# Kernel optimization log

Hardware: AMD Instinct MI355X
Metric: run time of the kernel (lower is better)

The kernel has to match this reference:

```python
import jax, jax.numpy as jnp
import numpy as np

MEM_DIM = 256
NUM_CHILDREN = 16
BATCH = 16384


def setup_inputs() -> dict:
    key = jax.random.key(0)
    k1, k2, k3, k4, k5, k6 = jax.random.split(key, 6)
    D = MEM_DIM
    s = 1.0 / np.sqrt(D)
    return {
        "children_memory": jax.random.normal(k1, (NUM_CHILDREN, BATCH, D), jnp.float32),
        "children_hidden": jax.random.normal(k2, (NUM_CHILDREN, BATCH, D), jnp.float32),
        "Wf": jax.random.normal(k3, (D, D), jnp.float32) * s,
        "bf": jax.random.normal(k4, (D,), jnp.float32) * s,
        "Wiou": jax.random.normal(k5, (3 * D, D), jnp.float32) * s,
        "biou": jax.random.normal(k6, (3 * D,), jnp.float32) * s,
    }


def reference(children_memory, children_hidden, Wf, bf, Wiou, biou):
    D = Wf.shape[0]
    # sum of children hidden states over the child axis -> [B, D]
    hidden_sum = jnp.sum(children_hidden, axis=0)
    # per-child forget gates: [C, B, D]
    forget_gates = jax.nn.sigmoid(jnp.einsum("cbd,ed->cbe", children_hidden, Wf) + bf)
    # i/o/u gates from summed hidden: [B, 3D]
    iou = jnp.einsum("bd,ed->be", hidden_sum, Wiou) + biou
    input_gate = jax.nn.sigmoid(iou[:, :D])
    output_gate = jax.nn.sigmoid(iou[:, D:2 * D])
    memory_gate = jnp.tanh(iou[:, 2 * D:])
    node_memory = input_gate * memory_gate + jnp.sum(forget_gates * children_memory, axis=0)
    node_hidden = output_gate * jnp.tanh(node_memory)
    return node_memory, node_hidden
```

## Files before the change

kernel.cpp:

```cpp
#include <hip/hip_runtime.h>
#include <hip/hip_bf16.h>

#define CC 16
#define BB 16384
#define DD 256
#define BT 16
#define NT 512
#define SLAB ((size_t)BB * DD)

typedef float f32x4 __attribute__((ext_vector_type(4)));
typedef short bf16x8 __attribute__((ext_vector_type(8)));
typedef short bf16x4 __attribute__((ext_vector_type(4)));

static __device__ __forceinline__ short bfc(float f) {
    return (short)__builtin_bit_cast(unsigned short, __float2bfloat16(f));
}
static __device__ __forceinline__ bf16x8 pack8(f32x4 a, f32x4 b) {
    bf16x8 v;
    v[0] = bfc(a[0]); v[1] = bfc(a[1]); v[2] = bfc(a[2]); v[3] = bfc(a[3]);
    v[4] = bfc(b[0]); v[5] = bfc(b[1]); v[6] = bfc(b[2]); v[7] = bfc(b[3]);
    return v;
}
static __device__ __forceinline__ float sigm(float x) {
    return __builtin_amdgcn_rcpf(1.0f + __expf(-x));
}
static __device__ __forceinline__ float tanh_(float x) {
    return 2.0f * __builtin_amdgcn_rcpf(1.0f + __expf(-2.0f * x)) - 1.0f;
}

__global__ void prep(const float* __restrict__ Wf, const float* __restrict__ Wiou,
                     short* __restrict__ ws) {
    const int row = blockIdx.x;
    const int t   = threadIdx.x;
    const float* src = (row < 256) ? (Wf + (size_t)row * DD)
                                   : (Wiou + (size_t)(row - 256) * DD);
    f32x4 v = *(const f32x4*)(src + t * 4);
    bf16x4 o; o[0] = bfc(v[0]); o[1] = bfc(v[1]); o[2] = bfc(v[2]); o[3] = bfc(v[3]);
    *(bf16x4*)(ws + (size_t)row * DD + t * 4) = o;
}

__global__ __launch_bounds__(NT, 2) void treelstm(
    const float* __restrict__ cmem,
    const float* __restrict__ chid,
    const short* __restrict__ wpk,
    const float* __restrict__ bfv,
    const float* __restrict__ biou,
    float* __restrict__ out)
{
    __shared__ __align__(64) unsigned char hb[2][2][BT * DD * 2];

    const int tid  = threadIdx.x;
    const int lane = tid & 63;
    const int wid  = tid >> 6;
    const int l15  = lane & 15;
    const int l4   = lane >> 4;
    const int b0   = blockIdx.x * BT;
    const int wc0  = wid * 32;
    const int swr  = l15 << 4;

    const int srow   = tid >> 5;
    const int schunk = tid & 31;
    const float* hg  = chid + (size_t)(b0 + srow) * DD + schunk * 8;
    const int wb     = srow * 512 + (((schunk ^ srow) & 31) << 4);

    f32x4 hA0 = *(const f32x4*)(hg);
    f32x4 hA1 = *(const f32x4*)(hg + 4);
    f32x4 hA2 = *(const f32x4*)(hg + SLAB);
    f32x4 hA3 = *(const f32x4*)(hg + SLAB + 4);

    bf16x8 wfr[2][8];
    float bfr[2];
#pragma unroll
    for (int n = 0; n < 2; ++n) {
        const short* wr = wpk + (size_t)(wc0 + n * 16 + l15) * DD + l4 * 8;
#pragma unroll
        for (int k = 0; k < 8; ++k) wfr[n][k] = *(const bf16x8*)(wr + k * 32);
        bfr[n] = bfv[wc0 + n * 16 + l15];
    }

    const float* cmp = cmem + (size_t)(b0 + l4 * 4) * DD + wc0 + l15;
    float cmE[8], cmO[8];
#pragma unroll
    for (int n = 0; n < 2; ++n)
#pragma unroll
        for (int j = 0; j < 4; ++j) cmE[n * 4 + j] = cmp[j * DD + n * 16];

    float hs[8], nmv[8];
#pragma unroll
    for (int i = 0; i < 8; ++i) { hs[i] = 0.f; nmv[i] = 0.f; }

#pragma unroll
    for (int i = 0; i < 4; ++i) {
        hs[i] += hA0[i] + hA2[i];
        hs[4 + i] += hA1[i] + hA3[i];
    }
    *(bf16x8*)(&hb[0][0][0] + wb) = pack8(hA0, hA1);
    *(bf16x8*)(&hb[0][1][0] + wb) = pack8(hA2, hA3);
    asm volatile("s_waitcnt lgkmcnt(0)" ::: "memory");
    __builtin_amdgcn_s_barrier();
    __builtin_amdgcn_sched_barrier(0);

    const float* hgn = hg + 2 * SLAB;
    const float* cmn = cmp + SLAB;

#pragma unroll 1
    for (int P = 0; P < 8; ++P) {
        if (P < 7) {
            hA0 = *(const f32x4*)(hgn);
            hA1 = *(const f32x4*)(hgn + 4);
            hA2 = *(const f32x4*)(hgn + SLAB);
            hA3 = *(const f32x4*)(hgn + SLAB + 4);
            hgn += 2 * SLAB;
        }
#pragma unroll
        for (int n = 0; n < 2; ++n)
#pragma unroll
            for (int j = 0; j < 4; ++j) cmO[n * 4 + j] = cmn[j * DD + n * 16];
        cmn += SLAB;

        f32x4 e0 = {bfr[0], bfr[0], bfr[0], bfr[0]};
        f32x4 e1 = {bfr[1], bfr[1], bfr[1], bfr[1]};
        f32x4 e2 = {0.f, 0.f, 0.f, 0.f}, e3 = {0.f, 0.f, 0.f, 0.f};
        const unsigned char* bcE = &hb[P & 1][0][0] + l15 * 512;
#pragma unroll
        for (int kk = 0; kk < 4; ++kk) {
            bf16x8 a = *(const bf16x8*)(bcE + ((((kk) << 6) + (l4 << 4)) ^ swr));
            e0 = __builtin_amdgcn_mfma_f32_16x16x32_bf16(a, wfr[0][kk], e0, 0, 0, 0);
            e1 = __builtin_amdgcn_mfma_f32_16x16x32_bf16(a, wfr[1][kk], e1, 0, 0, 0);
        }
#pragma unroll
        for (int kk = 4; kk < 8; ++kk) {
            bf16x8 a = *(const bf16x8*)(bcE + ((((kk) << 6) + (l4 << 4)) ^ swr));
            e2 = __builtin_amdgcn_mfma_f32_16x16x32_bf16(a, wfr[0][kk], e2, 0, 0, 0);
            e3 = __builtin_amdgcn_mfma_f32_16x16x32_bf16(a, wfr[1][kk], e3, 0, 0, 0);
        }
#pragma unroll
        for (int j = 0; j < 4; ++j) {
            nmv[j]     += sigm(e0[j] + e2[j]) * cmE[j];
            nmv[4 + j] += sigm(e1[j] + e3[j]) * cmE[4 + j];
        }
        if (P < 7) {
#pragma unroll
            for (int n = 0; n < 2; ++n)
#pragma unroll
                for (int j = 0; j < 4; ++j) cmE[n * 4 + j] = cmn[j * DD + n * 16];
        }
        cmn += SLAB;

        f32x4 o0 = {bfr[0], bfr[0], bfr[0], bfr[0]};
        f32x4 o1 = {bfr[1], bfr[1], bfr[1], bfr[1]};
        f32x4 o2 = {0.f, 0.f, 0.f, 0.f}, o3 = {0.f, 0.f, 0.f, 0.f};
        const unsigned char* bcO = &hb[P & 1][1][0] + l15 * 512;
#pragma unroll
        for (int kk = 0; kk < 4; ++kk) {
            bf16x8 a = *(const bf16x8*)(bcO + ((((kk) << 6) + (l4 << 4)) ^ swr));
            o0 = __builtin_amdgcn_mfma_f32_16x16x32_bf16(a, wfr[0][kk], o0, 0, 0, 0);
            o1 = __builtin_amdgcn_mfma_f32_16x16x32_bf16(a, wfr[1][kk], o1, 0, 0, 0);
        }
#pragma unroll
        for (int kk = 4; kk < 8; ++kk) {
            bf16x8 a = *(const bf16x8*)(bcO + ((((kk) << 6) + (l4 << 4)) ^ swr));
            o2 = __builtin_amdgcn_mfma_f32_16x16x32_bf16(a, wfr[0][kk], o2, 0, 0, 0);
            o3 = __builtin_amdgcn_mfma_f32_16x16x32_bf16(a, wfr[1][kk], o3, 0, 0, 0);
        }

        if (P < 7) {
#pragma unroll
            for (int i = 0; i < 4; ++i) {
                hs[i] += hA0[i] + hA2[i];
                hs[4 + i] += hA1[i] + hA3[i];
            }
            *(bf16x8*)(&hb[(P & 1) ^ 1][0][0] + wb) = pack8(hA0, hA1);
            *(bf16x8*)(&hb[(P & 1) ^ 1][1][0] + wb) = pack8(hA2, hA3);
            asm volatile("s_waitcnt lgkmcnt(0)" ::: "memory");
            __builtin_amdgcn_s_barrier();
            __builtin_amdgcn_sched_barrier(0);
        }

#pragma unroll
        for (int j = 0; j < 4; ++j) {
            nmv[j]     += sigm(o0[j] + o2[j]) * cmO[j];
            nmv[4 + j] += sigm(o1[j] + o3[j]) * cmO[4 + j];
        }
    }

    {
        f32x4 s0 = {hs[0], hs[1], hs[2], hs[3]};
        f32x4 s1 = {hs[4], hs[5], hs[6], hs[7]};
        *(bf16x8*)(&hb[0][0][0] + wb) = pack8(s0, s1);
    }
    asm volatile("s_waitcnt lgkmcnt(0)" ::: "memory");
    __builtin_amdgcn_s_barrier();
    __builtin_amdgcn_sched_barrier(0);

    bf16x8 afr[8];
    {
        const unsigned char* bc = &hb[0][0][0] + l15 * 512;
#pragma unroll
        for (int kk = 0; kk < 8; ++kk)
            afr[kk] = *(const bf16x8*)(bc + (((kk << 6) + (l4 << 4)) ^ swr));
    }

    float gq[3][8];
#pragma unroll
    for (int q = 0; q < 3; ++q) {
#pragma unroll
        for (int n = 0; n < 2; ++n) {
            const short* wr = wpk + (size_t)(256 + q * 256 + wc0 + n * 16 + l15) * DD + l4 * 8;
            f32x4 acc = {0.f, 0.f, 0.f, 0.f};
#pragma unroll
            for (int kk = 0; kk < 8; ++kk)
                acc = __builtin_amdgcn_mfma_f32_16x16x32_bf16(afr[kk], *(const bf16x8*)(wr + kk * 32), acc, 0, 0, 0);
            float bq = biou[q * 256 + wc0 + n * 16 + l15];
#pragma unroll
            for (int j = 0; j < 4; ++j) gq[q][n * 4 + j] = acc[j] + bq;
        }
    }

    float* o0p = out + (size_t)(b0 + l4 * 4) * DD + wc0 + l15;
    float* o1p = o0p + SLAB;
#pragma unroll
    for (int n = 0; n < 2; ++n)
#pragma unroll
        for (int j = 0; j < 4; ++j) {
            float ig = sigm(gq[0][n * 4 + j]);
            float og = sigm(gq[1][n * 4 + j]);
            float ug = tanh_(gq[2][n * 4 + j]);
            float mm = nmv[n * 4 + j] + ig * ug;
            float hh = og * tanh_(mm);
            o0p[j * DD + n * 16] = mm;
            o1p[j * DD + n * 16] = hh;
        }
}

extern "C" void kernel_launch(void* const* d_in, const int* in_sizes, int n_in,
                              void* d_out, int out_size, void* d_ws, size_t ws_size,
                              hipStream_t stream) {
    const float* cmem = (const float*)d_in[0];
    const float* chid = (const float*)d_in[1];
    const float* Wf   = (const float*)d_in[2];
    const float* bf   = (const float*)d_in[3];
    const float* Wiou = (const float*)d_in[4];
    const float* biou = (const float*)d_in[5];
    float* out = (float*)d_out;
    short* wpk = (short*)d_ws;

    prep<<<1024, 64, 0, stream>>>(Wf, Wiou, wpk);
    treelstm<<<BB / BT, NT, 0, stream>>>(cmem, chid, wpk, bf, biou, out);
}
```

Measured before the change: 165.1 us.

## Split output columns across two blocks per batch tile with 256 threads

Each batch tile of 16 rows is now processed by two blocks, each covering 128 of the 256 output columns with 4 waves instead of 8. Each block still stages the full hidden rows into shared memory, so children_hidden reads are duplicated across the pair. The odd-child hidden load is deferred to mid-iteration to reduce live registers. The aim is more blocks and occupancy flexibility, at the cost of doubled hidden-state traffic unless L2 absorbs it.

```diff
diff --git a/kernel.cpp b/kernel.cpp
--- a/kernel.cpp
+++ b/kernel.cpp
@@ -5,7 +5,7 @@
 #define BB 16384
 #define DD 256
 #define BT 16
-#define NT 512
+#define NT 256
 #define SLAB ((size_t)BB * DD)
 
 typedef float f32x4 __attribute__((ext_vector_type(4)));
@@ -54,83 +54,97 @@
     const int wid  = tid >> 6;
     const int l15  = lane & 15;
     const int l4   = lane >> 4;
-    const int b0   = blockIdx.x * BT;
-    const int wc0  = wid * 32;
-    const int swr  = l15 << 4;
-
-    const int srow   = tid >> 5;
-    const int schunk = tid & 31;
-    const float* hg  = chid + (size_t)(b0 + srow) * DD + schunk * 8;
-    const int wb     = srow * 512 + (((schunk ^ srow) & 31) << 4);
-
-    f32x4 hA0 = *(const f32x4*)(hg);
-    f32x4 hA1 = *(const f32x4*)(hg + 4);
-    f32x4 hA2 = *(const f32x4*)(hg + SLAB);
-    f32x4 hA3 = *(const f32x4*)(hg + SLAB + 4);
+    const int bx   = blockIdx.x;
+    const int b0   = (bx >> 1) * BT;
+    const int cbase = (bx & 1) * 128 + wid * 32;
+
+    const int srow = tid >> 4;
+    const int sfc  = (tid & 15) * 16;
+    const float* hg = chid + (size_t)(b0 + srow) * DD + sfc;
+    const int c0w = (tid & 15) * 2;
+    const int wb0 = srow * 512 + ((((c0w)     ^ srow) & 31) << 4);
+    const int wb1 = srow * 512 + ((((c0w + 1) ^ srow) & 31) << 4);
+
+    f32x4 hN0 = *(const f32x4*)(hg);
+    f32x4 hN1 = *(const f32x4*)(hg + 4);
+    f32x4 hN2 = *(const f32x4*)(hg + 8);
+    f32x4 hN3 = *(const f32x4*)(hg + 12);
+    f32x4 hO0 = *(const f32x4*)(hg + SLAB);
+    f32x4 hO1 = *(const f32x4*)(hg + SLAB + 4);
+    f32x4 hO2 = *(const f32x4*)(hg + SLAB + 8);
+    f32x4 hO3 = *(const f32x4*)(hg + SLAB + 12);
 
     bf16x8 wfr[2][8];
     float bfr[2];
 #pragma unroll
     for (int n = 0; n < 2; ++n) {
-        const short* wr = wpk + (size_t)(wc0 + n * 16 + l15) * DD + l4 * 8;
+        const short* wr = wpk + (size_t)(cbase + n * 16 + l15) * DD + l4 * 8;
 #pragma unroll
         for (int k = 0; k < 8; ++k) wfr[n][k] = *(const bf16x8*)(wr + k * 32);
-        bfr[n] = bfv[wc0 + n * 16 + l15];
-    }
-
-    const float* cmp = cmem + (size_t)(b0 + l4 * 4) * DD + wc0 + l15;
+        bfr[n] = bfv[cbase + n * 16 + l15];
+    }
+
+    const float* cmp = cmem + (size_t)(b0 + l4 * 4) * DD + cbase + l15;
     float cmE[8], cmO[8];
 #pragma unroll
     for (int n = 0; n < 2; ++n)
 #pragma unroll
         for (int j = 0; j < 4; ++j) cmE[n * 4 + j] = cmp[j * DD + n * 16];
 
-    float hs[8], nmv[8];
-#pragma unroll
-    for (int i = 0; i < 8; ++i) { hs[i] = 0.f; nmv[i] = 0.f; }
+    float hs[16], nmv[8];
+#pragma unroll
+    for (int i = 0; i < 16; ++i) hs[i] = 0.f;
+#pragma unroll
+    for (int i = 0; i < 8; ++i) nmv[i] = 0.f;
 
 #pragma unroll
     for (int i = 0; i < 4; ++i) {
-        hs[i] += hA0[i] + hA2[i];
-        hs[4 + i] += hA1[i] + hA3[i];
-    }
-    *(bf16x8*)(&hb[0][0][0] + wb) = pack8(hA0, hA1);
-    *(bf16x8*)(&hb[0][1][0] + wb) = pack8(hA2, hA3);
+        hs[i]      += hN0[i] + hO0[i];
+        hs[4 + i]  += hN1[i] + hO1[i];
+        hs[8 + i]  += hN2[i] + hO2[i];
+        hs[12 + i] += hN3[i] + hO3[i];
+    }
+    *(bf16x8*)(&hb[0][0][0] + wb0) = pack8(hN0, hN1);
+    *(bf16x8*)(&hb[0][0][0] + wb1) = pack8(hN2, hN3);
+    *(bf16x8*)(&hb[0][1][0] + wb0) = pack8(hO0, hO1);
+    *(bf16x8*)(&hb[0][1][0] + wb1) = pack8(hO2, hO3);
     asm volatile("s_waitcnt lgkmcnt(0)" ::: "memory");
     __builtin_amdgcn_s_barrier();
     __builtin_amdgcn_sched_barrier(0);
 
-    const float* hgn = hg + 2 * SLAB;
-    const float* cmn = cmp + SLAB;
+    const int swr = l15 << 4;
 
 #pragma unroll 1
     for (int P = 0; P < 8; ++P) {
+        const int par = P & 1;
         if (P < 7) {
-            hA0 = *(const f32x4*)(hgn);
-            hA1 = *(const f32x4*)(hgn + 4);
-            hA2 = *(const f32x4*)(hgn + SLAB);
-            hA3 = *(const f32x4*)(hgn + SLAB + 4);
-            hgn += 2 * SLAB;
-        }
-#pragma unroll
-        for (int n = 0; n < 2; ++n)
-#pragma unroll
-            for (int j = 0; j < 4; ++j) cmO[n * 4 + j] = cmn[j * DD + n * 16];
-        cmn += SLAB;
+            const float* hn = hg + (size_t)(2 * P + 2) * SLAB;
+            hN0 = *(const f32x4*)(hn);
+            hN1 = *(const f32x4*)(hn + 4);
+            hN2 = *(const f32x4*)(hn + 8);
+            hN3 = *(const f32x4*)(hn + 12);
+        }
+        {
+            const float* cn = cmp + (size_t)(2 * P + 1) * SLAB;
+#pragma unroll
+            for (int n = 0; n < 2; ++n)
+#pragma unroll
+                for (int j = 0; j < 4; ++j) cmO[n * 4 + j] = cn[j * DD + n * 16];
+        }
 
         f32x4 e0 = {bfr[0], bfr[0], bfr[0], bfr[0]};
         f32x4 e1 = {bfr[1], bfr[1], bfr[1], bfr[1]};
         f32x4 e2 = {0.f, 0.f, 0.f, 0.f}, e3 = {0.f, 0.f, 0.f, 0.f};
-        const unsigned char* bcE = &hb[P & 1][0][0] + l15 * 512;
+        const unsigned char* bcE = &hb[par][0][0] + l15 * 512;
 #pragma unroll
         for (int kk = 0; kk < 4; ++kk) {
-            bf16x8 a = *(const bf16x8*)(bcE + ((((kk) << 6) + (l4 << 4)) ^ swr));
+            bf16x8 a = *(const bf16x8*)(bcE + (((kk << 6) + (l4 << 4)) ^ swr));
             e0 = __builtin_amdgcn_mfma_f32_16x16x32_bf16(a, wfr[0][kk], e0, 0, 0, 0);
             e1 = __builtin_amdgcn_mfma_f32_16x16x32_bf16(a, wfr[1][kk], e1, 0, 0, 0);
         }
 #pragma unroll
         for (int kk = 4; kk < 8; ++kk) {
-            bf16x8 a = *(const bf16x8*)(bcE + ((((kk) << 6) + (l4 << 4)) ^ swr));
+            bf16x8 a = *(const bf16x8*)(bcE + (((kk << 6) + (l4 << 4)) ^ swr));
             e2 = __builtin_amdgcn_mfma_f32_16x16x32_bf16(a, wfr[0][kk], e2, 0, 0, 0);
             e3 = __builtin_amdgcn_mfma_f32_16x16x32_bf16(a, wfr[1][kk], e3, 0, 0, 0);
         }
@@ -139,27 +153,40 @@
             nmv[j]     += sigm(e0[j] + e2[j]) * cmE[j];
             nmv[4 + j] += sigm(e1[j] + e3[j]) * cmE[4 + j];
         }
+
         if (P < 7) {
 #pragma unroll
+            for (int i = 0; i < 4; ++i) {
+                hs[i] += hN0[i]; hs[4 + i] += hN1[i];
+                hs[8 + i] += hN2[i]; hs[12 + i] += hN3[i];
+            }
+            *(bf16x8*)(&hb[par ^ 1][0][0] + wb0) = pack8(hN0, hN1);
+            *(bf16x8*)(&hb[par ^ 1][0][0] + wb1) = pack8(hN2, hN3);
+            const float* ho = hg + (size_t)(2 * P + 3) * SLAB;
+            hO0 = *(const f32x4*)(ho);
+            hO1 = *(const f32x4*)(ho + 4);
+            hO2 = *(const f32x4*)(ho + 8);
+            hO3 = *(const f32x4*)(ho + 12);
+            const float* cn = cmp + (size_t)(2 * P + 2) * SLAB;
+#pragma unroll
             for (int n = 0; n < 2; ++n)
 #pragma unroll
-                for (int j = 0; j < 4; ++j) cmE[n * 4 + j] = cmn[j * DD + n * 16];
-        }
-        cmn += SLAB;
+                for (int j = 0; j < 4; ++j) cmE[n * 4 + j] = cn[j * DD + n * 16];
+        }
 
         f32x4 o0 = {bfr[0], bfr[0], bfr[0], bfr[0]};
         f32x4 o1 = {bfr[1], bfr[1], bfr[1], bfr[1]};
         f32x4 o2 = {0.f, 0.f, 0.f, 0.f}, o3 = {0.f, 0.f, 0.f, 0.f};
-        const unsigned char* bcO = &hb[P & 1][1][0] + l15 * 512;
+        const unsigned char* bcO = &hb[par][1][0] + l15 * 512;
 #pragma unroll
         for (int kk = 0; kk < 4; ++kk) {
-            bf16x8 a = *(const bf16x8*)(bcO + ((((kk) << 6) + (l4 << 4)) ^ swr));
+            bf16x8 a = *(const bf16x8*)(bcO + (((kk << 6) + (l4 << 4)) ^ swr));
             o0 = __builtin_amdgcn_mfma_f32_16x16x32_bf16(a, wfr[0][kk], o0, 0, 0, 0);
             o1 = __builtin_amdgcn_mfma_f32_16x16x32_bf16(a, wfr[1][kk], o1, 0, 0, 0);
         }
 #pragma unroll
         for (int kk = 4; kk < 8; ++kk) {
-            bf16x8 a = *(const bf16x8*)(bcO + ((((kk) << 6) + (l4 << 4)) ^ swr));
+            bf16x8 a = *(const bf16x8*)(bcO + (((kk << 6) + (l4 << 4)) ^ swr));
             o2 = __builtin_amdgcn_mfma_f32_16x16x32_bf16(a, wfr[0][kk], o2, 0, 0, 0);
             o3 = __builtin_amdgcn_mfma_f32_16x16x32_bf16(a, wfr[1][kk], o3, 0, 0, 0);
         }
@@ -167,11 +194,11 @@
         if (P < 7) {
 #pragma unroll
             for (int i = 0; i < 4; ++i) {
-                hs[i] += hA0[i] + hA2[i];
-                hs[4 + i] += hA1[i] + hA3[i];
+                hs[i] += hO0[i]; hs[4 + i] += hO1[i];
+                hs[8 + i] += hO2[i]; hs[12 + i] += hO3[i];
             }
-            *(bf16x8*)(&hb[(P & 1) ^ 1][0][0] + wb) = pack8(hA0, hA1);
-            *(bf16x8*)(&hb[(P & 1) ^ 1][1][0] + wb) = pack8(hA2, hA3);
+            *(bf16x8*)(&hb[par ^ 1][1][0] + wb0) = pack8(hO0, hO1);
+            *(bf16x8*)(&hb[par ^ 1][1][0] + wb1) = pack8(hO2, hO3);
             asm volatile("s_waitcnt lgkmcnt(0)" ::: "memory");
             __builtin_amdgcn_s_barrier();
             __builtin_amdgcn_sched_barrier(0);
@@ -187,7 +214,10 @@
     {
         f32x4 s0 = {hs[0], hs[1], hs[2], hs[3]};
         f32x4 s1 = {hs[4], hs[5], hs[6], hs[7]};
-        *(bf16x8*)(&hb[0][0][0] + wb) = pack8(s0, s1);
+        f32x4 s2 = {hs[8], hs[9], hs[10], hs[11]};
+        f32x4 s3 = {hs[12], hs[13], hs[14], hs[15]};
+        *(bf16x8*)(&hb[0][0][0] + wb0) = pack8(s0, s1);
+        *(bf16x8*)(&hb[0][0][0] + wb1) = pack8(s2, s3);
     }
     asm volatile("s_waitcnt lgkmcnt(0)" ::: "memory");
     __builtin_amdgcn_s_barrier();
@@ -206,18 +236,18 @@
     for (int q = 0; q < 3; ++q) {
 #pragma unroll
         for (int n = 0; n < 2; ++n) {
-            const short* wr = wpk + (size_t)(256 + q * 256 + wc0 + n * 16 + l15) * DD + l4 * 8;
+            const short* wr = wpk + (size_t)(256 + q * 256 + cbase + n * 16 + l15) * DD + l4 * 8;
             f32x4 acc = {0.f, 0.f, 0.f, 0.f};
 #pragma unroll
             for (int kk = 0; kk < 8; ++kk)
                 acc = __builtin_amdgcn_mfma_f32_16x16x32_bf16(afr[kk], *(const bf16x8*)(wr + kk * 32), acc, 0, 0, 0);
-            float bq = biou[q * 256 + wc0 + n * 16 + l15];
+            float bq = biou[q * 256 + cbase + n * 16 + l15];
 #pragma unroll
             for (int j = 0; j < 4; ++j) gq[q][n * 4 + j] = acc[j] + bq;
         }
     }
 
-    float* o0p = out + (size_t)(b0 + l4 * 4) * DD + wc0 + l15;
+    float* o0p = out + (size_t)(b0 + l4 * 4) * DD + cbase + l15;
     float* o1p = o0p + SLAB;
 #pragma unroll
     for (int n = 0; n < 2; ++n)
@@ -246,5 +276,5 @@
     short* wpk = (short*)d_ws;
 
     prep<<<1024, 64, 0, stream>>>(Wf, Wiou, wpk);
-    treelstm<<<BB / BT, NT, 0, stream>>>(cmem, chid, wpk, bf, biou, out);
-}
+    treelstm<<<(BB / BT) * 2, NT, 0, stream>>>(cmem, chid, wpk, bf, biou, out);
+}
```

Measured after the change: 169.0 us. +2.4%, slower.

## Load hidden A-fragments directly into registers and split columns across two blocks

Applied to the files above, without the earlier changes.

Replaces the LDS-staged, barrier-synchronised double buffer for child hidden states with direct per-wave global loads. Each wave now packs the full 16x256 bf16 A operand in registers and processes one child per iteration without any block barriers. The grid doubles, with each 256-thread block covering half the output columns. The price is that every wave, and both column-half blocks, re-read the same hidden tile, which relies on L1/L2 to absorb the redundant traffic. Register pressure also rises from holding 64 floats of prefetched hidden data.

```diff
diff --git a/kernel.cpp b/kernel.cpp
--- a/kernel.cpp
+++ b/kernel.cpp
@@ -4,8 +4,7 @@
 #define CC 16
 #define BB 16384
 #define DD 256
-#define BT 16
-#define NT 512
+#define NT 256
 #define SLAB ((size_t)BB * DD)
 
 typedef float f32x4 __attribute__((ext_vector_type(4)));
@@ -47,158 +46,121 @@
     const float* __restrict__ biou,
     float* __restrict__ out)
 {
-    __shared__ __align__(64) unsigned char hb[2][2][BT * DD * 2];
+    __shared__ float hsbuf[16][264];
 
     const int tid  = threadIdx.x;
     const int lane = tid & 63;
     const int wid  = tid >> 6;
     const int l15  = lane & 15;
     const int l4   = lane >> 4;
-    const int b0   = blockIdx.x * BT;
-    const int wc0  = wid * 32;
-    const int swr  = l15 << 4;
-
-    const int srow   = tid >> 5;
-    const int schunk = tid & 31;
-    const float* hg  = chid + (size_t)(b0 + srow) * DD + schunk * 8;
-    const int wb     = srow * 512 + (((schunk ^ srow) & 31) << 4);
-
-    f32x4 hA0 = *(const f32x4*)(hg);
-    f32x4 hA1 = *(const f32x4*)(hg + 4);
-    f32x4 hA2 = *(const f32x4*)(hg + SLAB);
-    f32x4 hA3 = *(const f32x4*)(hg + SLAB + 4);
+    const int bx   = blockIdx.x;
+    const int b0   = (bx >> 1) * 16;
+    const int cbase = (bx & 1) * 128 + wid * 32;
+
+    const float* hA = chid + (size_t)(b0 + l15) * DD + l4 * 8;
+
+    f32x4 hv[16];
+#pragma unroll
+    for (int kk = 0; kk < 8; ++kk) {
+        hv[2 * kk]     = *(const f32x4*)(hA + kk * 32);
+        hv[2 * kk + 1] = *(const f32x4*)(hA + kk * 32 + 4);
+    }
 
     bf16x8 wfr[2][8];
     float bfr[2];
 #pragma unroll
     for (int n = 0; n < 2; ++n) {
-        const short* wr = wpk + (size_t)(wc0 + n * 16 + l15) * DD + l4 * 8;
+        const short* wr = wpk + (size_t)(cbase + n * 16 + l15) * DD + l4 * 8;
 #pragma unroll
         for (int k = 0; k < 8; ++k) wfr[n][k] = *(const bf16x8*)(wr + k * 32);
-        bfr[n] = bfv[wc0 + n * 16 + l15];
-    }
-
-    const float* cmp = cmem + (size_t)(b0 + l4 * 4) * DD + wc0 + l15;
-    float cmE[8], cmO[8];
+        bfr[n] = bfv[cbase + n * 16 + l15];
+    }
+
+    const float* cmp = cmem + (size_t)(b0 + l4 * 4) * DD + cbase + l15;
+    float cmv[8];
 #pragma unroll
     for (int n = 0; n < 2; ++n)
 #pragma unroll
-        for (int j = 0; j < 4; ++j) cmE[n * 4 + j] = cmp[j * DD + n * 16];
-
-    float hs[8], nmv[8];
-#pragma unroll
-    for (int i = 0; i < 8; ++i) { hs[i] = 0.f; nmv[i] = 0.f; }
-
-#pragma unroll
-    for (int i = 0; i < 4; ++i) {
-        hs[i] += hA0[i] + hA2[i];
-        hs[4 + i] += hA1[i] + hA3[i];
-    }
-    *(bf16x8*)(&hb[0][0][0] + wb) = pack8(hA0, hA1);
-    *(bf16x8*)(&hb[0][1][0] + wb) = pack8(hA2, hA3);
-    asm volatile("s_waitcnt lgkmcnt(0)" ::: "memory");
-    __builtin_amdgcn_s_barrier();
-    __builtin_amdgcn_sched_barrier(0);
-
-    const float* hgn = hg + 2 * SLAB;
-    const float* cmn = cmp + SLAB;
+        for (int j = 0; j < 4; ++j) cmv[n * 4 + j] = cmp[j * DD + n * 16];
+
+    float hs[16], nmv[8];
+#pragma unroll
+    for (int i = 0; i < 16; ++i) hs[i] = 0.f;
+#pragma unroll
+    for (int i = 0; i < 8; ++i) nmv[i] = 0.f;
+
+    bf16x8 a[8];
 
 #pragma unroll 1
-    for (int P = 0; P < 8; ++P) {
-        if (P < 7) {
-            hA0 = *(const f32x4*)(hgn);
-            hA1 = *(const f32x4*)(hgn + 4);
-            hA2 = *(const f32x4*)(hgn + SLAB);
-            hA3 = *(const f32x4*)(hgn + SLAB + 4);
-            hgn += 2 * SLAB;
-        }
-#pragma unroll
-        for (int n = 0; n < 2; ++n)
-#pragma unroll
-            for (int j = 0; j < 4; ++j) cmO[n * 4 + j] = cmn[j * DD + n * 16];
-        cmn += SLAB;
-
-        f32x4 e0 = {bfr[0], bfr[0], bfr[0], bfr[0]};
-        f32x4 e1 = {bfr[1], bfr[1], bfr[1], bfr[1]};
-        f32x4 e2 = {0.f, 0.f, 0.f, 0.f}, e3 = {0.f, 0.f, 0.f, 0.f};
-        const unsigned char* bcE = &hb[P & 1][0][0] + l15 * 512;
-#pragma unroll
-        for (int kk = 0; kk < 4; ++kk) {
-            bf16x8 a = *(const bf16x8*)(bcE + ((((kk) << 6) + (l4 << 4)) ^ swr));
-            e0 = __builtin_amdgcn_mfma_f32_16x16x32_bf16(a, wfr[0][kk], e0, 0, 0, 0);
-            e1 = __builtin_amdgcn_mfma_f32_16x16x32_bf16(a, wfr[1][kk], e1, 0, 0, 0);
-        }
-#pragma unroll
-        for (int kk = 4; kk < 8; ++kk) {
-            bf16x8 a = *(const bf16x8*)(bcE + ((((kk) << 6) + (l4 << 4)) ^ swr));
-            e2 = __builtin_amdgcn_mfma_f32_16x16x32_bf16(a, wfr[0][kk], e2, 0, 0, 0);
-            e3 = __builtin_amdgcn_mfma_f32_16x16x32_bf16(a, wfr[1][kk], e3, 0, 0, 0);
-        }
+    for (int c = 0; c < CC; ++c) {
+#pragma unroll
+        for (int kk = 0; kk < 8; ++kk) {
+            if ((kk >> 1) == wid) {
+                const int half = (kk & 1) * 8;
+#pragma unroll
+                for (int i = 0; i < 4; ++i) {
+                    hs[half + i]     += hv[2 * kk][i];
+                    hs[half + 4 + i] += hv[2 * kk + 1][i];
+                }
+            }
+            a[kk] = pack8(hv[2 * kk], hv[2 * kk + 1]);
+        }
+
+        if (c + 1 < CC) {
+            const float* hn = hA + (size_t)(c + 1) * SLAB;
+#pragma unroll
+            for (int kk = 0; kk < 8; ++kk) {
+                hv[2 * kk]     = *(const f32x4*)(hn + kk * 32);
+                hv[2 * kk + 1] = *(const f32x4*)(hn + kk * 32 + 4);
+            }
+        }
+        float cmn[8];
+        if (c + 1 < CC) {
+            const float* cn = cmp + (size_t)(c + 1) * SLAB;
+#pragma unroll
+            for (int n = 0; n < 2; ++n)
+#pragma unroll
+                for (int j = 0; j < 4; ++j) cmn[n * 4 + j] = cn[j * DD + n * 16];
+        }
+
+        f32x4 acc0 = {bfr[0], bfr[0], bfr[0], bfr[0]};
+        f32x4 acc1 = {bfr[1], bfr[1], bfr[1], bfr[1]};
+#pragma unroll
+        for (int kk = 0; kk < 8; ++kk) {
+            acc0 = __builtin_amdgcn_mfma_f32_16x16x32_bf16(a[kk], wfr[0][kk], acc0, 0, 0, 0);
+            acc1 = __builtin_amdgcn_mfma_f32_16x16x32_bf16(a[kk], wfr[1][kk], acc1, 0, 0, 0);
+        }
+
 #pragma unroll
         for (int j = 0; j < 4; ++j) {
-            nmv[j]     += sigm(e0[j] + e2[j]) * cmE[j];
-            nmv[4 + j] += sigm(e1[j] + e3[j]) * cmE[4 + j];
-        }
-        if (P < 7) {
-#pragma unroll
-            for (int n = 0; n < 2; ++n)
-#pragma unroll
-                for (int j = 0; j < 4; ++j) cmE[n * 4 + j] = cmn[j * DD + n * 16];
-        }
-        cmn += SLAB;
-
-        f32x4 o0 = {bfr[0], bfr[0], bfr[0], bfr[0]};
-        f32x4 o1 = {bfr[1], bfr[1], bfr[1], bfr[1]};
-        f32x4 o2 = {0.f, 0.f, 0.f, 0.f}, o3 = {0.f, 0.f, 0.f, 0.f};
-        const unsigned char* bcO = &hb[P & 1][1][0] + l15 * 512;
-#pragma unroll
-        for (int kk = 0; kk < 4; ++kk) {
-            bf16x8 a = *(const bf16x8*)(bcO + ((((kk) << 6) + (l4 << 4)) ^ swr));
-            o0 = __builtin_amdgcn_mfma_f32_16x16x32_bf16(a, wfr[0][kk], o0, 0, 0, 0);
-            o1 = __builtin_amdgcn_mfma_f32_16x16x32_bf16(a, wfr[1][kk], o1, 0, 0, 0);
-        }
-#pragma unroll
-        for (int kk = 4; kk < 8; ++kk) {
-            bf16x8 a = *(const bf16x8*)(bcO + ((((kk) << 6) + (l4 << 4)) ^ swr));
-            o2 = __builtin_amdgcn_mfma_f32_16x16x32_bf16(a, wfr[0][kk], o2, 0, 0, 0);
-            o3 = __builtin_amdgcn_mfma_f32_16x16x32_bf16(a, wfr[1][kk], o3, 0, 0, 0);
-        }
-
-        if (P < 7) {
-#pragma unroll
-            for (int i = 0; i < 4; ++i) {
-                hs[i] += hA0[i] + hA2[i];
-                hs[4 + i] += hA1[i] + hA3[i];
-            }
-            *(bf16x8*)(&hb[(P & 1) ^ 1][0][0] + wb) = pack8(hA0, hA1);
-            *(bf16x8*)(&hb[(P & 1) ^ 1][1][0] + wb) = pack8(hA2, hA3);
-            asm volatile("s_waitcnt lgkmcnt(0)" ::: "memory");
-            __builtin_amdgcn_s_barrier();
-            __builtin_amdgcn_sched_barrier(0);
-        }
-
-#pragma unroll
-        for (int j = 0; j < 4; ++j) {
-            nmv[j]     += sigm(o0[j] + o2[j]) * cmO[j];
-            nmv[4 + j] += sigm(o1[j] + o3[j]) * cmO[4 + j];
+            nmv[j]     += sigm(acc0[j]) * cmv[j];
+            nmv[4 + j] += sigm(acc1[j]) * cmv[4 + j];
+        }
+        if (c + 1 < CC) {
+#pragma unroll
+            for (int i = 0; i < 8; ++i) cmv[i] = cmn[i];
         }
     }
 
     {
+        float* p0 = &hsbuf[l15][(2 * wid) * 32 + l4 * 8];
         f32x4 s0 = {hs[0], hs[1], hs[2], hs[3]};
         f32x4 s1 = {hs[4], hs[5], hs[6], hs[7]};
-        *(bf16x8*)(&hb[0][0][0] + wb) = pack8(s0, s1);
-    }
-    asm volatile("s_waitcnt lgkmcnt(0)" ::: "memory");
-    __builtin_amdgcn_s_barrier();
-    __builtin_amdgcn_sched_barrier(0);
+        f32x4 s2 = {hs[8], hs[9], hs[10], hs[11]};
+        f32x4 s3 = {hs[12], hs[13], hs[14], hs[15]};
+        *(f32x4*)(p0)      = s0;
+        *(f32x4*)(p0 + 4)  = s1;
+        *(f32x4*)(p0 + 32) = s2;
+        *(f32x4*)(p0 + 36) = s3;
+    }
+    __syncthreads();
 
     bf16x8 afr[8];
-    {
-        const unsigned char* bc = &hb[0][0][0] + l15 * 512;
-#pragma unroll
-        for (int kk = 0; kk < 8; ++kk)
-            afr[kk] = *(const bf16x8*)(bc + (((kk << 6) + (l4 << 4)) ^ swr));
+#pragma unroll
+    for (int kk = 0; kk < 8; ++kk) {
+        f32x4 x0 = *(const f32x4*)(&hsbuf[l15][kk * 32 + l4 * 8]);
+        f32x4 x1 = *(const f32x4*)(&hsbuf[l15][kk * 32 + l4 * 8 + 4]);
+        afr[kk] = pack8(x0, x1);
     }
 
     float gq[3][8];
@@ -206,18 +168,18 @@
     for (int q = 0; q < 3; ++q) {
 #pragma unroll
         for (int n = 0; n < 2; ++n) {
-            const short* wr = wpk + (size_t)(256 + q * 256 + wc0 + n * 16 + l15) * DD + l4 * 8;
+            const short* wr = wpk + (size_t)(256 + q * 256 + cbase + n * 16 + l15) * DD + l4 * 8;
             f32x4 acc = {0.f, 0.f, 0.f, 0.f};
 #pragma unroll
             for (int kk = 0; kk < 8; ++kk)
                 acc = __builtin_amdgcn_mfma_f32_16x16x32_bf16(afr[kk], *(const bf16x8*)(wr + kk * 32), acc, 0, 0, 0);
-            float bq = biou[q * 256 + wc0 + n * 16 + l15];
+            float bq = biou[q * 256 + cbase + n * 16 + l15];
 #pragma unroll
             for (int j = 0; j < 4; ++j) gq[q][n * 4 + j] = acc[j] + bq;
         }
     }
 
-    float* o0p = out + (size_t)(b0 + l4 * 4) * DD + wc0 + l15;
+    float* o0p = out + (size_t)(b0 + l4 * 4) * DD + cbase + l15;
     float* o1p = o0p + SLAB;
 #pragma unroll
     for (int n = 0; n < 2; ++n)
@@ -246,5 +208,5 @@
     short* wpk = (short*)d_ws;
 
     prep<<<1024, 64, 0, stream>>>(Wf, Wiou, wpk);
-    treelstm<<<BB / BT, NT, 0, stream>>>(cmem, chid, wpk, bf, biou, out);
-}
+    treelstm<<<(BB / 16) * 2, NT, 0, stream>>>(cmem, chid, wpk, bf, biou, out);
+}
```

Measured after the change: 412.8 us. +150.0%, slower.
